# Performance work log

Measured on AMD Instinct MI355X. Metric: run time of the kernel, lower is better.

The kernel has to match this reference:

```python
import jax, jax.numpy as jnp
import numpy as np

D_MODEL = 1024
NUM_HEADS = 16
DEPTH = D_MODEL // NUM_HEADS
B, S = 2, 2048


def setup_inputs() -> dict:
    key = jax.random.key(0)
    ks = jax.random.split(key, 12)
    scale = 1.0 / np.sqrt(D_MODEL)
    inp = {
        "Q": jax.random.normal(ks[0], (B, S, D_MODEL), jnp.float32),
        "K": jax.random.normal(ks[1], (B, S, D_MODEL), jnp.float32),
        "V": jax.random.normal(ks[2], (B, S, D_MODEL), jnp.float32),
        "mask": jnp.zeros((B, 1, 1, S), jnp.float32),  # 1.0 = masked, 0.0 = attend
        "Wq": jax.random.normal(ks[3], (D_MODEL, D_MODEL), jnp.float32) * scale,
        "bq": jnp.zeros((D_MODEL,), jnp.float32),
        "Wk": jax.random.normal(ks[4], (D_MODEL, D_MODEL), jnp.float32) * scale,
        "bk": jnp.zeros((D_MODEL,), jnp.float32),
        "Wv": jax.random.normal(ks[5], (D_MODEL, D_MODEL), jnp.float32) * scale,
        "bv": jnp.zeros((D_MODEL,), jnp.float32),
        "Wo": jax.random.normal(ks[6], (D_MODEL, D_MODEL), jnp.float32) * scale,
        "bo": jnp.zeros((D_MODEL,), jnp.float32),
    }
    return inp


def _split_heads(x):
    b, s, _ = x.shape
    return x.reshape(b, s, NUM_HEADS, DEPTH).transpose(0, 2, 1, 3)  # [b,h,s,d]


def reference(Q, K, V, mask, Wq, bq, Wk, bk, Wv, bv, Wo, bo):
    q = _split_heads(Q @ Wq + bq)
    k = _split_heads(K @ Wk + bk)
    v = _split_heads(V @ Wv + bv)
    scores = jnp.einsum("bhqd,bhkd->bhqk", q, k) / jnp.sqrt(jnp.float32(DEPTH))
    scores = scores + mask * -1e9
    attn = jax.nn.softmax(scores, axis=-1)  # [b,h,q,k]
    out = jnp.einsum("bhqk,bhkd->bhqd", attn, v)
    out = out.transpose(0, 2, 1, 3).reshape(Q.shape[0], -1, D_MODEL)
    out = out @ Wo + bo
    return out, attn
```

## Files before the change

kernel.cpp:

```cpp
#include <hip/hip_runtime.h>

#define D_MODEL 1024
#define NHEADS  16
#define DEPTH   64
#define BB      2
#define SS      2048
#define MROWS   (BB*SS)
#define BHN     (BB*NHEADS)

using f16 = _Float16;
using f16x4 = __attribute__((ext_vector_type(4))) _Float16;
using f16x8 = __attribute__((ext_vector_type(8))) _Float16;
using f32x4 = __attribute__((ext_vector_type(4))) float;

__device__ __forceinline__ void g2l16(const void* g, void* l) {
  __builtin_amdgcn_global_load_lds(
      (const __attribute__((address_space(1))) void*)g,
      (__attribute__((address_space(3))) void*)l, 16, 0, 0);
}

__global__ __launch_bounds__(256) void cast_qkv(
    const float* __restrict__ Q, const float* __restrict__ K,
    const float* __restrict__ V, f16* __restrict__ dst) {
  const float* src = blockIdx.z == 0 ? Q : blockIdx.z == 1 ? K : V;
  f16* d = dst + (size_t)blockIdx.z * MROWS * D_MODEL;
  const size_t i = ((size_t)blockIdx.x * 256 + threadIdx.x) * 8;
  const float4 a = *(const float4*)(src + i);
  const float4 b = *(const float4*)(src + i + 4);
  f16x8 o;
  o[0] = (f16)a.x; o[1] = (f16)a.y; o[2] = (f16)a.z; o[3] = (f16)a.w;
  o[4] = (f16)b.x; o[5] = (f16)b.y; o[6] = (f16)b.z; o[7] = (f16)b.w;
  *(f16x8*)(d + i) = o;
}

__global__ __launch_bounds__(256) void wtrans(
    const float* __restrict__ w0, const float* __restrict__ w1,
    const float* __restrict__ w2, const float* __restrict__ w3,
    f16* __restrict__ wt) {
  const float* W = blockIdx.z == 0 ? w0 : blockIdx.z == 1 ? w1 : blockIdx.z == 2 ? w2 : w3;
  f16* Wt = wt + (size_t)blockIdx.z * D_MODEL * D_MODEL;
  __shared__ float tile[64][65];
  const int t = threadIdx.x;
  const int bx = blockIdx.x * 64, by = blockIdx.y * 64;
  const int c = t & 63, r0 = t >> 6;
#pragma unroll
  for (int i = 0; i < 16; ++i) {
    int r = r0 + i * 4;
    tile[r][c] = W[(size_t)(by + r) * D_MODEL + bx + c];
  }
  __syncthreads();
#pragma unroll
  for (int i = 0; i < 16; ++i) {
    int r = r0 + i * 4;
    Wt[(size_t)(bx + r) * D_MODEL + by + c] = (f16)tile[c][r];
  }
}

__global__ __launch_bounds__(256) void proj_gemm(
    const f16* __restrict__ qkv16, const f16* __restrict__ Wt,
    const float* __restrict__ bq, const float* __restrict__ bk, const float* __restrict__ bv,
    f16* __restrict__ heads) {
  const int z = blockIdx.z;
  const f16* A = qkv16 + (size_t)z * MROWS * D_MODEL;
  const f16* Bt = Wt + (size_t)z * D_MODEL * D_MODEL;
  const float* bias = z == 0 ? bq : z == 1 ? bk : bv;
  f16* dst = heads + (size_t)z * MROWS * D_MODEL;

  __shared__ f16 As[128 * 64];
  __shared__ f16 Bs[128 * 64];
  const int t = threadIdx.x, lane = t & 63, w = t >> 6;
  const int l15 = lane & 15, g = lane >> 4;
  const int m0 = blockIdx.y * 128, n0 = blockIdx.x * 128;
  const int wr = (w >> 1) * 64, wc = (w & 1) * 64;
  f32x4 acc[4][4] = {};

  for (int k0 = 0; k0 < D_MODEL; k0 += 64) {
    __syncthreads();
#pragma unroll
    for (int i = 0; i < 4; ++i) {
      int seg = t + i * 256;
      int row = seg >> 3, c8 = (seg & 7) * 8;
      g2l16(A  + (size_t)(m0 + row) * D_MODEL + k0 + c8, &As[seg * 8]);
      g2l16(Bt + (size_t)(n0 + row) * D_MODEL + k0 + c8, &Bs[seg * 8]);
    }
    __syncthreads();
#pragma unroll
    for (int kk = 0; kk < 2; ++kk) {
      f16x8 af[4], bfr[4];
#pragma unroll
      for (int i = 0; i < 4; ++i)
        af[i] = *(const f16x8*)&As[(wr + i * 16 + l15) * 64 + kk * 32 + g * 8];
#pragma unroll
      for (int j = 0; j < 4; ++j)
        bfr[j] = *(const f16x8*)&Bs[(wc + j * 16 + l15) * 64 + kk * 32 + g * 8];
#pragma unroll
      for (int i = 0; i < 4; ++i)
#pragma unroll
        for (int j = 0; j < 4; ++j)
          acc[i][j] = __builtin_amdgcn_mfma_f32_16x16x32_f16(af[i], bfr[j], acc[i][j], 0, 0, 0);
    }
  }
#pragma unroll
  for (int i = 0; i < 4; ++i)
#pragma unroll
    for (int j = 0; j < 4; ++j) {
      int n = n0 + wc + j * 16 + l15;
      float bn = bias[n];
      int h = n >> 6, d = n & 63;
#pragma unroll
      for (int r = 0; r < 4; ++r) {
        int m = m0 + wr + i * 16 + g * 4 + r;
        int b = m >> 11, s = m & 2047;
        dst[((size_t)(b * NHEADS + h) * SS + s) * DEPTH + d] = (f16)(acc[i][j][r] + bn);
      }
    }
}

__global__ __launch_bounds__(256) void vtrans(
    const f16* __restrict__ vh, f16* __restrict__ vt) {
  const int bh = blockIdx.y;
  const int n0 = blockIdx.x * 128;
  const f16* src = vh + (size_t)bh * SS * DEPTH;
  f16* dst = vt + (size_t)bh * DEPTH * SS;
  __shared__ f16 tile[128][72];
  const int t = threadIdx.x;
#pragma unroll
  for (int iss = 0; iss < 4; ++iss) {
    int seg = t + iss * 256;
    int n = seg >> 3, c = seg & 7;
    *(f16x8*)&tile[n][c * 8] = *(const f16x8*)(src + (size_t)(n0 + n) * DEPTH + c * 8);
  }
  __syncthreads();
#pragma unroll
  for (int iss = 0; iss < 4; ++iss) {
    int seg = t + iss * 256;
    int d = seg >> 4, c = seg & 15;
    f16x8 v;
#pragma unroll
    for (int e = 0; e < 8; ++e) v[e] = tile[c * 8 + e][d];
    *(f16x8*)(dst + (size_t)d * SS + n0 + c * 8) = v;
  }
}

__global__ __launch_bounds__(256) void attn_fused(
    const f16* __restrict__ qh, const f16* __restrict__ kh,
    const f16* __restrict__ vt, const float* __restrict__ mask,
    float* __restrict__ attn, f16* __restrict__ outh) {
  const int bh = blockIdx.y, b = bh >> 4, h = bh & 15;
  const int m0 = blockIdx.x * 128;
  const f16* Kb = kh + (size_t)bh * SS * DEPTH;
  const f16* Vb = vt + (size_t)bh * DEPTH * SS;
  const float* mB = mask + (size_t)b * SS;
  float* Ab = attn + (size_t)bh * SS * SS;

  __shared__ f16 Ks[2][128 * 64];
  __shared__ f16 Vs[2][64 * 128];

  const int t = threadIdx.x, lane = t & 63, w = t >> 6;
  const int l15 = lane & 15, g = lane >> 4;

  f16x8 bq[2][2];
  {
    const f16* Qb = qh + (size_t)bh * SS * DEPTH;
#pragma unroll
    for (int j = 0; j < 2; ++j)
#pragma unroll
      for (int kk = 0; kk < 2; ++kk)
        bq[j][kk] = *(const f16x8*)(Qb + (size_t)(m0 + w * 32 + j * 16 + l15) * DEPTH + kk * 32 + g * 8);
  }

  auto stageK = [&](int buf, int ct) {
#pragma unroll
    for (int iss = 0; iss < 4; ++iss) {
      int seg = t + iss * 256;
      int n = seg >> 3, c = seg & 7;
      int csrc = c ^ (n & 7);
      g2l16(Kb + (size_t)(ct * 128 + n) * DEPTH + csrc * 8, &Ks[buf][seg * 8]);
    }
  };
  auto stageV = [&](int buf, int ct) {
#pragma unroll
    for (int iss = 0; iss < 4; ++iss) {
      int seg = t + iss * 256;
      int d = seg >> 4, c = seg & 15;
      int csrc = c ^ ((d >> 1) & 7);
      g2l16(Vb + (size_t)d * SS + ct * 128 + csrc * 8, &Vs[buf][seg * 8]);
    }
  };
  auto qkStep = [&](const f16* ks, f32x4 (&accS)[8][2]) {
    __builtin_amdgcn_s_setprio(1);
#pragma unroll
    for (int kk = 0; kk < 2; ++kk) {
#pragma unroll
      for (int i = 0; i < 8; ++i) {
        int n = i * 16 + l15;
        int c = (g + 4 * kk) ^ (l15 & 7);
        f16x8 ak = *(const f16x8*)&ks[n * 64 + c * 8];
#pragma unroll
        for (int j = 0; j < 2; ++j)
          accS[i][j] = __builtin_amdgcn_mfma_f32_16x16x32_f16(ak, bq[j][kk], accS[i][j], 0, 0, 0);
      }
    }
    __builtin_amdgcn_s_setprio(0);
  };

  float rm[2] = {-3.0e38f, -3.0e38f}, rs[2] = {0.0f, 0.0f};
  stageK(0, 0);
  __syncthreads();
  for (int ct = 0; ct < 16; ++ct) {
    const int cur = ct & 1;
    if (ct < 15) stageK(cur ^ 1, ct + 1);
    f32x4 accS[8][2] = {};
    qkStep(Ks[cur], accS);
#pragma unroll
    for (int i = 0; i < 8; ++i) {
      const float4 m4 = *(const float4*)(mB + ct * 128 + i * 16 + g * 4);
      const float mv[4] = {m4.x * -1e9f, m4.y * -1e9f, m4.z * -1e9f, m4.w * -1e9f};
#pragma unroll
      for (int j = 0; j < 2; ++j)
#pragma unroll
        for (int r = 0; r < 4; ++r)
          accS[i][j][r] = accS[i][j][r] * 0.125f + mv[r];
    }
#pragma unroll
    for (int j = 0; j < 2; ++j) {
      float tm = -3.0e38f;
#pragma unroll
      for (int i = 0; i < 8; ++i)
        tm = fmaxf(tm, fmaxf(fmaxf(accS[i][j][0], accS[i][j][1]),
                             fmaxf(accS[i][j][2], accS[i][j][3])));
      tm = fmaxf(tm, __shfl_xor(tm, 16, 64));
      tm = fmaxf(tm, __shfl_xor(tm, 32, 64));
      const float mn = fmaxf(rm[j], tm);
      float ts = 0.0f;
#pragma unroll
      for (int i = 0; i < 8; ++i)
#pragma unroll
        for (int r = 0; r < 4; ++r)
          ts += __expf(accS[i][j][r] - mn);
      ts += __shfl_xor(ts, 16, 64);
      ts += __shfl_xor(ts, 32, 64);
      rs[j] = rs[j] * __expf(rm[j] - mn) + ts;
      rm[j] = mn;
    }
    __syncthreads();
  }

  const float invs[2] = {1.0f / rs[0], 1.0f / rs[1]};
  f32x4 accO[2][4] = {};
  stageK(0, 0); stageV(0, 0);
  __syncthreads();
  for (int ct = 0; ct < 16; ++ct) {
    const int cur = ct & 1;
    if (ct < 15) { stageK(cur ^ 1, ct + 1); stageV(cur ^ 1, ct + 1); }
    f32x4 accS[8][2] = {};
    qkStep(Ks[cur], accS);
    const f16* vs = Vs[cur];
#pragma unroll
    for (int i = 0; i < 8; ++i) {
      const float4 m4 = *(const float4*)(mB + ct * 128 + i * 16 + g * 4);
      const float mv[4] = {m4.x * -1e9f, m4.y * -1e9f, m4.z * -1e9f, m4.w * -1e9f};
      f16x4 bv[4];
#pragma unroll
      for (int df = 0; df < 4; ++df) {
        const int d = df * 16 + l15;
        const int c16 = 2 * i + (g >> 1);
        const int sw = c16 ^ ((d >> 1) & 7);
        bv[df] = *(const f16x4*)&vs[d * 128 + sw * 8 + (g & 1) * 4];
      }
#pragma unroll
      for (int j = 0; j < 2; ++j) {
        float p[4];
#pragma unroll
        for (int r = 0; r < 4; ++r)
          p[r] = __expf(accS[i][j][r] * 0.125f + mv[r] - rm[j]) * invs[j];
        float4 st; st.x = p[0]; st.y = p[1]; st.z = p[2]; st.w = p[3];
        *(float4*)(Ab + (size_t)(m0 + w * 32 + j * 16 + l15) * SS + ct * 128 + i * 16 + g * 4) = st;
        f16x4 pa; pa[0] = (f16)p[0]; pa[1] = (f16)p[1]; pa[2] = (f16)p[2]; pa[3] = (f16)p[3];
        __builtin_amdgcn_s_setprio(1);
#pragma unroll
        for (int df = 0; df < 4; ++df)
          accO[j][df] = __builtin_amdgcn_mfma_f32_16x16x16f16(pa, bv[df], accO[j][df], 0, 0, 0);
        __builtin_amdgcn_s_setprio(0);
      }
    }
    __syncthreads();
  }

  f16* Ob = outh + (size_t)b * SS * D_MODEL + h * DEPTH;
#pragma unroll
  for (int j = 0; j < 2; ++j)
#pragma unroll
    for (int df = 0; df < 4; ++df) {
      const int d = df * 16 + l15;
#pragma unroll
      for (int r = 0; r < 4; ++r) {
        const int s = m0 + w * 32 + j * 16 + g * 4 + r;
        Ob[(size_t)s * D_MODEL + d] = (f16)accO[j][df][r];
      }
    }
}

__global__ __launch_bounds__(256) void final_gemm(
    const f16* __restrict__ A, const f16* __restrict__ Bt,
    const float* __restrict__ bias, float* __restrict__ out) {
  __shared__ f16 As[128 * 64];
  __shared__ f16 Bs[128 * 64];
  const int t = threadIdx.x, lane = t & 63, w = t >> 6;
  const int l15 = lane & 15, g = lane >> 4;
  const int m0 = blockIdx.y * 128, n0 = blockIdx.x * 128;
  const int wr = (w >> 1) * 64, wc = (w & 1) * 64;
  f32x4 acc[4][4] = {};

  for (int k0 = 0; k0 < D_MODEL; k0 += 64) {
    __syncthreads();
#pragma unroll
    for (int i = 0; i < 4; ++i) {
      int seg = t + i * 256;
      int row = seg >> 3, c8 = (seg & 7) * 8;
      g2l16(A  + (size_t)(m0 + row) * D_MODEL + k0 + c8, &As[seg * 8]);
      g2l16(Bt + (size_t)(n0 + row) * D_MODEL + k0 + c8, &Bs[seg * 8]);
    }
    __syncthreads();
#pragma unroll
    for (int kk = 0; kk < 2; ++kk) {
      f16x8 af[4], bfr[4];
#pragma unroll
      for (int i = 0; i < 4; ++i)
        af[i] = *(const f16x8*)&As[(wr + i * 16 + l15) * 64 + kk * 32 + g * 8];
#pragma unroll
      for (int j = 0; j < 4; ++j)
        bfr[j] = *(const f16x8*)&Bs[(wc + j * 16 + l15) * 64 + kk * 32 + g * 8];
#pragma unroll
      for (int i = 0; i < 4; ++i)
#pragma unroll
        for (int j = 0; j < 4; ++j)
          acc[i][j] = __builtin_amdgcn_mfma_f32_16x16x32_f16(af[i], bfr[j], acc[i][j], 0, 0, 0);
    }
  }
#pragma unroll
  for (int i = 0; i < 4; ++i)
#pragma unroll
    for (int j = 0; j < 4; ++j) {
      int n = n0 + wc + j * 16 + l15;
      float bn = bias[n];
#pragma unroll
      for (int r = 0; r < 4; ++r) {
        int m = m0 + wr + i * 16 + g * 4 + r;
        out[(size_t)m * D_MODEL + n] = acc[i][j][r] + bn;
      }
    }
}

extern "C" void kernel_launch(void* const* d_in, const int* in_sizes, int n_in,
                              void* d_out, int out_size, void* d_ws, size_t ws_size,
                              hipStream_t stream) {
  const float* Q    = (const float*)d_in[0];
  const float* K    = (const float*)d_in[1];
  const float* V    = (const float*)d_in[2];
  const float* mask = (const float*)d_in[3];
  const float* Wq   = (const float*)d_in[4];
  const float* bq   = (const float*)d_in[5];
  const float* Wk   = (const float*)d_in[6];
  const float* bk   = (const float*)d_in[7];
  const float* Wv   = (const float*)d_in[8];
  const float* bv   = (const float*)d_in[9];
  const float* Wo   = (const float*)d_in[10];
  const float* bo   = (const float*)d_in[11];

  float* out0 = (float*)d_out;
  float* attn = out0 + (size_t)MROWS * D_MODEL;

  char* ws = (char*)d_ws;
  f16* Wt    = (f16*)ws;
  f16* heads = (f16*)(ws + (size_t)8 * 1024 * 1024);
  f16* outh  = (f16*)(ws + (size_t)32 * 1024 * 1024);
  f16* vtr   = (f16*)(ws + (size_t)40 * 1024 * 1024);
  f16* qh = heads;
  f16* kh = heads + (size_t)MROWS * D_MODEL;
  f16* vh = heads + (size_t)2 * MROWS * D_MODEL;

  f16* qkv16 = (f16*)attn;

  cast_qkv<<<dim3(2048, 1, 3), 256, 0, stream>>>(Q, K, V, qkv16);
  wtrans<<<dim3(16, 16, 4), 256, 0, stream>>>(Wq, Wk, Wv, Wo, Wt);
  proj_gemm<<<dim3(8, 32, 3), 256, 0, stream>>>(qkv16, Wt, bq, bk, bv, heads);
  vtrans<<<dim3(16, BHN), 256, 0, stream>>>(vh, vtr);
  attn_fused<<<dim3(16, BHN), 256, 0, stream>>>(qh, kh, vtr, mask, attn, outh);
  final_gemm<<<dim3(8, 32), 256, 0, stream>>>(outh, Wt + (size_t)3 * D_MODEL * D_MODEL, bo, out0);
}
```

Baseline: 880.4 us.

## Fuse fp32-to-fp16 input cast into projection GEMM and drop setprio hints

Removes the separate cast_qkv kernel and has proj_gemm read fp32 Q/K/V directly, converting to fp16 while staging into LDS, with the A tile row stride padded to 80 halves. The aim is to cut the fp16 intermediate round trip and one launch. In exchange the A loads become synchronous register-staged loads instead of async global_load_lds, and the A matrix is re-read as fp32 by each of the 8 column blocks, doubling that traffic. The change also strips the s_setprio hints around the MFMA sections in the attention kernel.

After: 860.9 us. 2.2% less time.

```diff
diff --git a/kernel.cpp b/kernel.cpp
--- a/kernel.cpp
+++ b/kernel.cpp
@@ -17,20 +17,6 @@
   __builtin_amdgcn_global_load_lds(
       (const __attribute__((address_space(1))) void*)g,
       (__attribute__((address_space(3))) void*)l, 16, 0, 0);
-}
-
-__global__ __launch_bounds__(256) void cast_qkv(
-    const float* __restrict__ Q, const float* __restrict__ K,
-    const float* __restrict__ V, f16* __restrict__ dst) {
-  const float* src = blockIdx.z == 0 ? Q : blockIdx.z == 1 ? K : V;
-  f16* d = dst + (size_t)blockIdx.z * MROWS * D_MODEL;
-  const size_t i = ((size_t)blockIdx.x * 256 + threadIdx.x) * 8;
-  const float4 a = *(const float4*)(src + i);
-  const float4 b = *(const float4*)(src + i + 4);
-  f16x8 o;
-  o[0] = (f16)a.x; o[1] = (f16)a.y; o[2] = (f16)a.z; o[3] = (f16)a.w;
-  o[4] = (f16)b.x; o[5] = (f16)b.y; o[6] = (f16)b.z; o[7] = (f16)b.w;
-  *(f16x8*)(d + i) = o;
 }
 
 __global__ __launch_bounds__(256) void wtrans(
@@ -57,16 +43,17 @@
 }
 
 __global__ __launch_bounds__(256) void proj_gemm(
-    const f16* __restrict__ qkv16, const f16* __restrict__ Wt,
+    const float* __restrict__ Q, const float* __restrict__ K, const float* __restrict__ V,
+    const f16* __restrict__ Wt,
     const float* __restrict__ bq, const float* __restrict__ bk, const float* __restrict__ bv,
     f16* __restrict__ heads) {
   const int z = blockIdx.z;
-  const f16* A = qkv16 + (size_t)z * MROWS * D_MODEL;
+  const float* A = z == 0 ? Q : z == 1 ? K : V;
   const f16* Bt = Wt + (size_t)z * D_MODEL * D_MODEL;
   const float* bias = z == 0 ? bq : z == 1 ? bk : bv;
   f16* dst = heads + (size_t)z * MROWS * D_MODEL;
 
-  __shared__ f16 As[128 * 64];
+  __shared__ f16 As[128 * 80];
   __shared__ f16 Bs[128 * 64];
   const int t = threadIdx.x, lane = t & 63, w = t >> 6;
   const int l15 = lane & 15, g = lane >> 4;
@@ -77,10 +64,17 @@
   for (int k0 = 0; k0 < D_MODEL; k0 += 64) {
     __syncthreads();
 #pragma unroll
+    for (int i = 0; i < 8; ++i) {
+      int seg = t + i * 256;
+      int row = seg >> 4, c4 = (seg & 15) * 4;
+      const float4 v4 = *(const float4*)(A + (size_t)(m0 + row) * D_MODEL + k0 + c4);
+      f16x4 p; p[0] = (f16)v4.x; p[1] = (f16)v4.y; p[2] = (f16)v4.z; p[3] = (f16)v4.w;
+      *(f16x4*)&As[row * 80 + c4] = p;
+    }
+#pragma unroll
     for (int i = 0; i < 4; ++i) {
       int seg = t + i * 256;
       int row = seg >> 3, c8 = (seg & 7) * 8;
-      g2l16(A  + (size_t)(m0 + row) * D_MODEL + k0 + c8, &As[seg * 8]);
       g2l16(Bt + (size_t)(n0 + row) * D_MODEL + k0 + c8, &Bs[seg * 8]);
     }
     __syncthreads();
@@ -89,7 +83,7 @@
       f16x8 af[4], bfr[4];
 #pragma unroll
       for (int i = 0; i < 4; ++i)
-        af[i] = *(const f16x8*)&As[(wr + i * 16 + l15) * 64 + kk * 32 + g * 8];
+        af[i] = *(const f16x8*)&As[(wr + i * 16 + l15) * 80 + kk * 32 + g * 8];
 #pragma unroll
       for (int j = 0; j < 4; ++j)
         bfr[j] = *(const f16x8*)&Bs[(wc + j * 16 + l15) * 64 + kk * 32 + g * 8];
@@ -188,7 +182,6 @@
     }
   };
   auto qkStep = [&](const f16* ks, f32x4 (&accS)[8][2]) {
-    __builtin_amdgcn_s_setprio(1);
 #pragma unroll
     for (int kk = 0; kk < 2; ++kk) {
 #pragma unroll
@@ -201,7 +194,6 @@
           accS[i][j] = __builtin_amdgcn_mfma_f32_16x16x32_f16(ak, bq[j][kk], accS[i][j], 0, 0, 0);
       }
     }
-    __builtin_amdgcn_s_setprio(0);
   };
 
   float rm[2] = {-3.0e38f, -3.0e38f}, rs[2] = {0.0f, 0.0f};
@@ -277,11 +269,9 @@
         float4 st; st.x = p[0]; st.y = p[1]; st.z = p[2]; st.w = p[3];
         *(float4*)(Ab + (size_t)(m0 + w * 32 + j * 16 + l15) * SS + ct * 128 + i * 16 + g * 4) = st;
         f16x4 pa; pa[0] = (f16)p[0]; pa[1] = (f16)p[1]; pa[2] = (f16)p[2]; pa[3] = (f16)p[3];
-        __builtin_amdgcn_s_setprio(1);
 #pragma unroll
         for (int df = 0; df < 4; ++df)
           accO[j][df] = __builtin_amdgcn_mfma_f32_16x16x16f16(pa, bv[df], accO[j][df], 0, 0, 0);
-        __builtin_amdgcn_s_setprio(0);
       }
     }
     __syncthreads();
@@ -380,11 +370,8 @@
   f16* kh = heads + (size_t)MROWS * D_MODEL;
   f16* vh = heads + (size_t)2 * MROWS * D_MODEL;
 
-  f16* qkv16 = (f16*)attn;
-
-  cast_qkv<<<dim3(2048, 1, 3), 256, 0, stream>>>(Q, K, V, qkv16);
   wtrans<<<dim3(16, 16, 4), 256, 0, stream>>>(Wq, Wk, Wv, Wo, Wt);
-  proj_gemm<<<dim3(8, 32, 3), 256, 0, stream>>>(qkv16, Wt, bq, bk, bv, heads);
+  proj_gemm<<<dim3(8, 32, 3), 256, 0, stream>>>(Q, K, V, Wt, bq, bk, bv, heads);
   vtrans<<<dim3(16, BHN), 256, 0, stream>>>(vh, vtr);
   attn_fused<<<dim3(16, BHN), 256, 0, stream>>>(qh, kh, vtr, mask, attn, outh);
   final_gemm<<<dim3(8, 32), 256, 0, stream>>>(outh, Wt + (size_t)3 * D_MODEL * D_MODEL, bo, out0);
```
